# Kernel tuning notes

Measured on AMD Instinct MI355X. Metric: run time of the kernel, lower is better.

Reference implementation:

```python
import jax, jax.numpy as jnp
import numpy as np

B, L, IN_DIM, D_MODEL, N_LAYERS = 4, 1024, 64, 512, 3
D_INNER, STATE, DT_RANK, K = 1024, 16, 32, 4  # expand=2, dt_rank=d_model//16, conv kernel 4


def setup_inputs() -> dict:
    key = jax.random.key(0)
    ks = jax.random.split(key, 8)
    s = 0.02
    def rn(k, shp):
        return jax.random.normal(k, shp, jnp.float32) * s
    inp = {"x": jax.random.normal(ks[0], (B, L, IN_DIM), jnp.float32)}
    inp["input_w"] = rn(ks[1], (D_MODEL, IN_DIM)); inp["input_b"] = jnp.zeros((D_MODEL,), jnp.float32)
    inp["in_proj_w"] = rn(ks[2], (N_LAYERS, 2 * D_INNER, D_MODEL)); inp["in_proj_b"] = jnp.zeros((N_LAYERS, 2 * D_INNER), jnp.float32)
    inp["conv_w"] = rn(ks[3], (N_LAYERS, D_INNER, 1, K)); inp["conv_b"] = jnp.zeros((N_LAYERS, D_INNER), jnp.float32)
    inp["x_proj_w"] = rn(ks[4], (N_LAYERS, DT_RANK + 2 * STATE, D_INNER))
    inp["dt_proj_w"] = rn(ks[5], (N_LAYERS, D_INNER, DT_RANK)); inp["dt_proj_b"] = jnp.full((N_LAYERS, D_INNER), -4.0, jnp.float32)
    inp["A_log"] = jnp.tile(jnp.log(jnp.arange(1, STATE + 1, dtype=jnp.float32))[None, None, :], (N_LAYERS, D_INNER, 1))
    inp["D"] = jnp.ones((N_LAYERS, D_INNER), jnp.float32)
    inp["out_proj_w"] = rn(ks[6], (N_LAYERS, D_MODEL, D_INNER)); inp["out_proj_b"] = jnp.zeros((N_LAYERS, D_MODEL), jnp.float32)
    inp["ln_w"] = jnp.ones((N_LAYERS, D_MODEL), jnp.float32); inp["ln_b"] = jnp.zeros((N_LAYERS, D_MODEL), jnp.float32)
    return inp


def _layernorm(x, w, b):
    mu = jnp.mean(x, -1, keepdims=True)
    v = jnp.var(x, -1, keepdims=True)
    return (x - mu) * jax.lax.rsqrt(v + 1e-5) * w + b


def _mamba(u, iw, ib, cw, cb, xw, dw, db, A_log, Dp, ow, ob):
    # u: [B, L, d_model]
    xz = u @ iw.T + ib                          # [B, L, 2*d_inner]
    xp, z = jnp.split(xz, 2, axis=-1)
    # causal depthwise conv over time
    xc = jax.lax.conv_general_dilated(xp.transpose(0, 2, 1), cw, (1,), [(K - 1, 0)],
                                      feature_group_count=D_INNER,
                                      dimension_numbers=("NCH", "OIH", "NCH")) + cb[None, :, None]
    xc = jax.nn.silu(xc).transpose(0, 2, 1)     # [B, L, d_inner]
    proj = xc @ xw.T                            # [B, L, dt_rank + 2*N]
    dtl = proj[..., :DT_RANK]
    Bm = proj[..., DT_RANK:DT_RANK + STATE]
    Cm = proj[..., DT_RANK + STATE:]
    dt = jax.nn.softplus(dtl @ dw.T + db)       # [B, L, d_inner]
    A = -jnp.exp(A_log)                         # [d_inner, N]

    def step(h, t):
        dt_t, B_t, C_t, x_t = t                 # [B,d], [B,N], [B,N], [B,d]
        h = h * jnp.exp(dt_t[..., None] * A) + (dt_t * x_t)[..., None] * B_t[:, None, :]
        return h, jnp.einsum("bdn,bn->bd", h, C_t)

    h0 = jnp.zeros((u.shape[0], D_INNER, STATE), u.dtype)
    _, ys = jax.lax.scan(step, h0, (dt.transpose(1, 0, 2), Bm.transpose(1, 0, 2),
                                    Cm.transpose(1, 0, 2), xc.transpose(1, 0, 2)))
    y = ys.transpose(1, 0, 2) + xc * Dp
    y = y * jax.nn.silu(z)
    return y @ ow.T + ob


def reference(x, input_w, input_b, in_proj_w, in_proj_b, conv_w, conv_b, x_proj_w,
              dt_proj_w, dt_proj_b, A_log, D, out_proj_w, out_proj_b, ln_w, ln_b):
    h = x @ input_w.T + input_b                 # [B, L, d_model]
    for i in range(N_LAYERS):
        res = h
        h = _mamba(h, in_proj_w[i], in_proj_b[i], conv_w[i], conv_b[i], x_proj_w[i],
                   dt_proj_w[i], dt_proj_b[i], A_log[i], D[i], out_proj_w[i], out_proj_b[i])
        h = _layernorm(h + res, ln_w[i], ln_b[i])
    return h[:, -1, :]
```

## Files before the change

kernel.cpp:

```cpp
#include <hip/hip_runtime.h>
#include <hip/hip_bf16.h>
#include <cstddef>
#include <cstdint>

#define NB 4
#define NL 1024
#define IN_DIM 64
#define D_MODEL 512
#define N_LAYERS 3
#define D_INNER 1024
#define NSTATE 16
#define DT_RANK 32
#define KCONV 4
#define NROWS (NB * NL)
#define CHUNK 16
#define NCHUNK (NL / CHUNK)
#define LOG2E 1.4426950408889634f

typedef __attribute__((ext_vector_type(8))) short short8;
typedef __attribute__((ext_vector_type(4))) float f32x4;
typedef __attribute__((ext_vector_type(4))) unsigned short us4;
typedef unsigned short ushort_t;

__device__ __forceinline__ ushort_t f2b1(float x) {
  uint32_t u = __builtin_bit_cast(uint32_t, x);
  u += 0x7fffu + ((u >> 16) & 1u);
  return (ushort_t)(u >> 16);
}

__global__ __launch_bounds__(256) void f2b_kernel(
    const float* __restrict__ in, ushort_t* __restrict__ out, int n)
{
  const int i = (blockIdx.x * 256 + threadIdx.x) * 4;
  if (i >= n) return;
  const float4 v = *(const float4*)(in + i);
  us4 o;
  o.x = f2b1(v.x); o.y = f2b1(v.y); o.z = f2b1(v.z); o.w = f2b1(v.w);
  *(us4*)(out + i) = o;
}

template<int BM, int BN, int MF, int NF, int ACT, bool WF32, bool WB16>
__global__ __launch_bounds__(256) void gemm_mfma(
    const ushort_t* __restrict__ A, int lda,
    const ushort_t* __restrict__ W,
    const float* __restrict__ bias,
    float* __restrict__ Cf, ushort_t* __restrict__ Cb,
    int M, int N, int K)
{
  constexpr int LDSK = 48;
  constexpr int CA = BM / 64;
  constexpr int CB = BN / 64;
  __shared__ __align__(16) short sa[BM * LDSK];
  __shared__ __align__(16) short sb[BN * LDSK];

  const int tid = threadIdx.x;
  const int l = tid & 63;
  const int wid = tid >> 6;
  const int wrow = (wid >> 1) * (BM / 2);
  const int wcol = (wid & 1) * (BN / 2);
  const int m0 = blockIdx.y * BM;
  const int n0 = blockIdx.x * BN;

  f32x4 acc[MF][NF] = {};
  short8 ra[CA], rb[CB];

  auto loadg = [&](int k0) {
#pragma unroll
    for (int c = 0; c < CA; ++c) {
      const int chunk = c * 256 + tid;
      const int row = chunk >> 2, colb = chunk & 3;
      ra[c] = *(const short8*)(A + (size_t)(m0 + row) * lda + k0 + colb * 8);
    }
#pragma unroll
    for (int c = 0; c < CB; ++c) {
      const int chunk = c * 256 + tid;
      const int row = chunk >> 2, colb = chunk & 3;
      rb[c] = *(const short8*)(W + (size_t)(n0 + row) * K + k0 + colb * 8);
    }
  };
  auto store_lds = [&]() {
#pragma unroll
    for (int c = 0; c < CA; ++c) {
      const int chunk = c * 256 + tid;
      *(short8*)(sa + (chunk >> 2) * LDSK + (chunk & 3) * 8) = ra[c];
    }
#pragma unroll
    for (int c = 0; c < CB; ++c) {
      const int chunk = c * 256 + tid;
      *(short8*)(sb + (chunk >> 2) * LDSK + (chunk & 3) * 8) = rb[c];
    }
  };

  loadg(0);
  for (int k0 = 0; k0 < K; k0 += 32) {
    __syncthreads();
    store_lds();
    __syncthreads();
    if (k0 + 32 < K) loadg(k0 + 32);

    short8 af[MF], bfr[NF];
#pragma unroll
    for (int mi = 0; mi < MF; ++mi)
      af[mi] = *(const short8*)(sa + (wrow + mi * 16 + (l & 15)) * LDSK + (l >> 4) * 8);
#pragma unroll
    for (int nj = 0; nj < NF; ++nj)
      bfr[nj] = *(const short8*)(sb + (wcol + nj * 16 + (l & 15)) * LDSK + (l >> 4) * 8);
#pragma unroll
    for (int mi = 0; mi < MF; ++mi)
#pragma unroll
      for (int nj = 0; nj < NF; ++nj)
        acc[mi][nj] = __builtin_amdgcn_mfma_f32_16x16x32_bf16(
            af[mi], bfr[nj], acc[mi][nj], 0, 0, 0);
  }

#pragma unroll
  for (int nj = 0; nj < NF; ++nj) {
    const int col = n0 + wcol + nj * 16 + (l & 15);
    const float bv = bias ? bias[col] : 0.f;
#pragma unroll
    for (int mi = 0; mi < MF; ++mi) {
#pragma unroll
      for (int q = 0; q < 4; ++q) {
        const int row = m0 + wrow + mi * 16 + (l >> 4) * 4 + q;
        float v = acc[mi][nj][q] + bv;
        if (ACT == 1) v = (v > 20.f) ? v : log1pf(__expf(v));
        if (WF32) Cf[(size_t)row * N + col] = v;
        if (WB16) Cb[(size_t)row * N + col] = f2b1(v);
      }
    }
  }
}

__global__ __launch_bounds__(256) void conv_silu(
    const float* __restrict__ xz,
    const float* __restrict__ cw,
    const float* __restrict__ cb,
    float* __restrict__ xc,
    ushort_t* __restrict__ xcb)
{
  const int idx = blockIdx.x * 256 + threadIdx.x;
  const int d = idx & (D_INNER - 1);
  const int bt = idx >> 10;
  const int t = bt & (NL - 1);
  const int b = bt >> 10;

  float accv = cb[d];
#pragma unroll
  for (int j = 0; j < KCONV; ++j) {
    const int tt = t - (KCONV - 1) + j;
    if (tt >= 0)
      accv = fmaf(xz[((size_t)(b * NL + tt)) * (2 * D_INNER) + d], cw[d * KCONV + j], accv);
  }
  const float sig = 1.f / (1.f + __expf(-accv));
  const float val = accv * sig;
  xc[idx] = val;
  xcb[idx] = f2b1(val);
}

__global__ __launch_bounds__(256) void scan_phase1(
    const float* __restrict__ dt,
    const float* __restrict__ proj,
    const float* __restrict__ xc,
    const float* __restrict__ A_log,
    float* __restrict__ S_loc,
    float* __restrict__ sumdt)
{
  const int d = blockIdx.x * 256 + threadIdx.x;
  const int c = blockIdx.y;
  const int b = blockIdx.z;

  float A2[NSTATE];
#pragma unroll
  for (int n = 0; n < NSTATE; ++n)
    A2[n] = -__expf(A_log[d * NSTATE + n]) * LOG2E;

  float h[NSTATE];
#pragma unroll
  for (int n = 0; n < NSTATE; ++n) h[n] = 0.f;
  float sdt = 0.f;

  const int t0 = c * CHUNK;
#pragma unroll 4
  for (int tt = 0; tt < CHUNK; ++tt) {
    const size_t row = (size_t)(b * NL + t0 + tt);
    const float dtv = dt[row * D_INNER + d];
    const float xv = xc[row * D_INNER + d];
    const float* pr = proj + row * (DT_RANK + 2 * NSTATE);
    sdt += dtv;
    const float dx = dtv * xv;
#pragma unroll
    for (int n = 0; n < NSTATE; ++n)
      h[n] = fmaf(h[n], exp2f(dtv * A2[n]), dx * pr[DT_RANK + n]);
  }

  const size_t cbase = (size_t)(b * NCHUNK + c);
  sumdt[cbase * D_INNER + d] = sdt;
#pragma unroll
  for (int n = 0; n < NSTATE; ++n)
    S_loc[(cbase * NSTATE + n) * D_INNER + d] = h[n];
}

__global__ __launch_bounds__(256) void scan_carry(
    const float* __restrict__ S_loc,
    const float* __restrict__ sumdt,
    const float* __restrict__ A_log,
    float* __restrict__ H_in)
{
  const int idx = blockIdx.x * 256 + threadIdx.x;
  const int d = idx & (D_INNER - 1);
  const int n = (idx >> 10) & (NSTATE - 1);
  const int b = idx >> 14;

  const float A2n = -__expf(A_log[d * NSTATE + n]) * LOG2E;

  float H = 0.f;
  for (int c = 0; c < NCHUNK; ++c) {
    const size_t cbase = (size_t)(b * NCHUNK + c);
    H_in[(cbase * NSTATE + n) * D_INNER + d] = H;
    const float sdt = sumdt[cbase * D_INNER + d];
    H = fmaf(H, exp2f(A2n * sdt), S_loc[(cbase * NSTATE + n) * D_INNER + d]);
  }
}

__global__ __launch_bounds__(256) void scan_phase2(
    const float* __restrict__ dt,
    const float* __restrict__ proj,
    const float* __restrict__ xz,
    const float* __restrict__ A_log,
    const float* __restrict__ Dp,
    const float* __restrict__ H_in,
    const float* __restrict__ xc,
    ushort_t* __restrict__ yb)
{
  const int d = blockIdx.x * 256 + threadIdx.x;
  const int c = blockIdx.y;
  const int b = blockIdx.z;

  float A2[NSTATE];
#pragma unroll
  for (int n = 0; n < NSTATE; ++n)
    A2[n] = -__expf(A_log[d * NSTATE + n]) * LOG2E;

  const size_t cbase = (size_t)(b * NCHUNK + c);
  float h[NSTATE];
#pragma unroll
  for (int n = 0; n < NSTATE; ++n)
    h[n] = H_in[(cbase * NSTATE + n) * D_INNER + d];

  const float Dv = Dp[d];
  const int t0 = c * CHUNK;

#pragma unroll 4
  for (int tt = 0; tt < CHUNK; ++tt) {
    const size_t row = (size_t)(b * NL + t0 + tt);
    const size_t rd = row * D_INNER + d;
    const float dtv = dt[rd];
    const float xv = xc[rd];
    const float* pr = proj + row * (DT_RANK + 2 * NSTATE);
    const float dx = dtv * xv;
    float accv = 0.f;
#pragma unroll
    for (int n = 0; n < NSTATE; ++n) {
      h[n] = fmaf(h[n], exp2f(dtv * A2[n]), dx * pr[DT_RANK + n]);
      accv = fmaf(h[n], pr[DT_RANK + NSTATE + n], accv);
    }
    const float zv = xz[row * (2 * D_INNER) + D_INNER + d];
    float yv = fmaf(xv, Dv, accv);
    yv *= zv / (1.f + __expf(-zv));
    yb[rd] = f2b1(yv);
  }
}

__global__ __launch_bounds__(256) void add_ln(
    const float* __restrict__ x,
    const float* __restrict__ res,
    const float* __restrict__ w,
    const float* __restrict__ bln,
    float* __restrict__ out,
    ushort_t* __restrict__ outb)
{
  const int wave = threadIdx.x >> 6;
  const int lane = threadIdx.x & 63;
  const int row = blockIdx.x * 4 + wave;
  const float* xr = x + (size_t)row * D_MODEL;
  const float* rr = res + (size_t)row * D_MODEL;

  float v[8];
  float s = 0.f, s2 = 0.f;
#pragma unroll
  for (int i = 0; i < 8; ++i) {
    const float t = xr[lane + i * 64] + rr[lane + i * 64];
    v[i] = t; s += t; s2 = fmaf(t, t, s2);
  }
#pragma unroll
  for (int off = 32; off; off >>= 1) {
    s += __shfl_xor(s, off);
    s2 += __shfl_xor(s2, off);
  }
  const float mean = s * (1.f / D_MODEL);
  const float var = s2 * (1.f / D_MODEL) - mean * mean;
  const float rstd = rsqrtf(var + 1e-5f);
#pragma unroll
  for (int i = 0; i < 8; ++i) {
    const int c = lane + i * 64;
    const float o = (v[i] - mean) * rstd * w[c] + bln[c];
    out[(size_t)row * D_MODEL + c] = o;
    outb[(size_t)row * D_MODEL + c] = f2b1(o);
  }
}

__global__ __launch_bounds__(256) void extract_last(
    const float* __restrict__ h, float* __restrict__ out)
{
  const int idx = blockIdx.x * 256 + threadIdx.x;
  if (idx < NB * D_MODEL) {
    const int b = idx >> 9, j = idx & (D_MODEL - 1);
    out[idx] = h[((size_t)(b * NL + NL - 1)) * D_MODEL + j];
  }
}

extern "C" void kernel_launch(void* const* d_in, const int* in_sizes, int n_in,
                              void* d_out, int out_size, void* d_ws, size_t ws_size,
                              hipStream_t stream)
{
  const float* x         = (const float*)d_in[0];
  const float* input_w   = (const float*)d_in[1];
  const float* input_b   = (const float*)d_in[2];
  const float* in_proj_w = (const float*)d_in[3];
  const float* in_proj_b = (const float*)d_in[4];
  const float* conv_w    = (const float*)d_in[5];
  const float* conv_b    = (const float*)d_in[6];
  const float* x_proj_w  = (const float*)d_in[7];
  const float* dt_proj_w = (const float*)d_in[8];
  const float* dt_proj_b = (const float*)d_in[9];
  const float* A_log     = (const float*)d_in[10];
  const float* Dp        = (const float*)d_in[11];
  const float* out_proj_w= (const float*)d_in[12];
  const float* out_proj_b= (const float*)d_in[13];
  const float* ln_w      = (const float*)d_in[14];
  const float* ln_b      = (const float*)d_in[15];

  float* p = (float*)d_ws;
  float* h0   = p; p += (size_t)NROWS * D_MODEL;
  float* h1   = p; p += (size_t)NROWS * D_MODEL;
  float* xz   = p; p += (size_t)NROWS * 2 * D_INNER;
  float* xc   = p; p += (size_t)NROWS * D_INNER;
  float* proj = p; p += (size_t)NROWS * 64;
  float* dtb  = p; p += (size_t)NROWS * D_INNER;
  float* Sloc = p; p += (size_t)NB * NCHUNK * NSTATE * D_INNER;
  float* Hin  = p; p += (size_t)NB * NCHUNK * NSTATE * D_INNER;
  float* sdt  = p; p += (size_t)NB * NCHUNK * D_INNER;
  ushort_t* hb    = (ushort_t*)p; p += (size_t)NROWS * D_MODEL / 2;
  ushort_t* xb    = (ushort_t*)p; p += (size_t)NROWS * IN_DIM / 2;
  ushort_t* projb = (ushort_t*)p; p += (size_t)NROWS * 64 / 2;
  ushort_t* inwb  = (ushort_t*)p; p += (size_t)D_MODEL * IN_DIM / 2;
  ushort_t* iwb   = (ushort_t*)p; p += (size_t)N_LAYERS * 2 * D_INNER * D_MODEL / 2;
  ushort_t* xwb   = (ushort_t*)p; p += (size_t)N_LAYERS * 64 * D_INNER / 2;
  ushort_t* dwb   = (ushort_t*)p; p += (size_t)N_LAYERS * D_INNER * DT_RANK / 2;
  ushort_t* owb   = (ushort_t*)p; p += (size_t)N_LAYERS * D_MODEL * D_INNER / 2;
  ushort_t* yb  = (ushort_t*)Sloc;
  ushort_t* xcb = (ushort_t*)Hin;
  float* tmp = xz;

  auto cvt = [&](const float* src, ushort_t* dst, int n) {
    f2b_kernel<<<(n / 4 + 255) / 256, 256, 0, stream>>>(src, dst, n);
  };
  cvt(x, xb, NROWS * IN_DIM);
  cvt(input_w, inwb, D_MODEL * IN_DIM);
  cvt(in_proj_w, iwb, N_LAYERS * 2 * D_INNER * D_MODEL);
  cvt(x_proj_w, xwb, N_LAYERS * 64 * D_INNER);
  cvt(dt_proj_w, dwb, N_LAYERS * D_INNER * DT_RANK);
  cvt(out_proj_w, owb, N_LAYERS * D_MODEL * D_INNER);

  gemm_mfma<64, 128, 2, 4, 0, true, true>
      <<<dim3(D_MODEL / 128, NROWS / 64), 256, 0, stream>>>(
      xb, IN_DIM, inwb, input_b, h0, hb, NROWS, D_MODEL, IN_DIM);

  float* hc = h0;
  float* hn = h1;

  for (int l = 0; l < N_LAYERS; ++l) {
    const ushort_t* iw = iwb + (size_t)l * 2 * D_INNER * D_MODEL;
    const float* ib = in_proj_b + (size_t)l * 2 * D_INNER;
    const float* cw = conv_w    + (size_t)l * D_INNER * KCONV;
    const float* cb = conv_b    + (size_t)l * D_INNER;
    const ushort_t* xw = xwb + (size_t)l * 64 * D_INNER;
    const ushort_t* dw = dwb + (size_t)l * D_INNER * DT_RANK;
    const float* db = dt_proj_b + (size_t)l * D_INNER;
    const float* Al = A_log     + (size_t)l * D_INNER * NSTATE;
    const float* Dl = Dp        + (size_t)l * D_INNER;
    const ushort_t* ow = owb + (size_t)l * D_MODEL * D_INNER;
    const float* ob = out_proj_b+ (size_t)l * D_MODEL;
    const float* lw = ln_w      + (size_t)l * D_MODEL;
    const float* lb = ln_b      + (size_t)l * D_MODEL;

    gemm_mfma<128, 128, 4, 4, 0, true, false>
        <<<dim3(2 * D_INNER / 128, NROWS / 128), 256, 0, stream>>>(
        hb, D_MODEL, iw, ib, xz, nullptr, NROWS, 2 * D_INNER, D_MODEL);

    conv_silu<<<NROWS * D_INNER / 256, 256, 0, stream>>>(xz, cw, cb, xc, xcb);

    gemm_mfma<64, 64, 2, 2, 0, true, true>
        <<<dim3(1, NROWS / 64), 256, 0, stream>>>(
        xcb, D_INNER, xw, nullptr, proj, projb, NROWS, 64, D_INNER);

    gemm_mfma<128, 128, 4, 4, 1, true, false>
        <<<dim3(D_INNER / 128, NROWS / 128), 256, 0, stream>>>(
        projb, 64, dw, db, dtb, nullptr, NROWS, D_INNER, DT_RANK);

    scan_phase1<<<dim3(D_INNER / 256, NCHUNK, NB), 256, 0, stream>>>(
        dtb, proj, xc, Al, Sloc, sdt);
    scan_carry<<<(NB * NSTATE * D_INNER) / 256, 256, 0, stream>>>(
        Sloc, sdt, Al, Hin);
    scan_phase2<<<dim3(D_INNER / 256, NCHUNK, NB), 256, 0, stream>>>(
        dtb, proj, xz, Al, Dl, Hin, xc, yb);

    gemm_mfma<64, 128, 2, 4, 0, true, false>
        <<<dim3(D_MODEL / 128, NROWS / 64), 256, 0, stream>>>(
        yb, D_INNER, ow, ob, tmp, nullptr, NROWS, D_MODEL, D_INNER);

    add_ln<<<NROWS / 4, 256, 0, stream>>>(tmp, hc, lw, lb, hn, hb);

    float* t2 = hc; hc = hn; hn = t2;
  }

  extract_last<<<(NB * D_MODEL + 255) / 256, 256, 0, stream>>>(hc, (float*)d_out);
}
```

Baseline: 578.0 us.

## Fuse scan kernels, store intermediates as bf16, use direct LDS loads in GEMM

Merges the three chunked-scan kernels into one block-level kernel that does the inter-chunk carry in shared memory. Stores xz, xc, dt and y as bf16 instead of fp32 and vectorizes the conv. The GEMM now uses global_load_lds into unpadded LDS and drops its register prefetch, the weight conversions become one kernel, and last-row extraction moves into layernorm. This reduces memory traffic and launch count, at the cost of lower intermediate precision and less load/compute overlap in the GEMM.

```diff
diff --git a/kernel.cpp b/kernel.cpp
--- a/kernel.cpp
+++ b/kernel.cpp
@@ -27,16 +27,45 @@
   u += 0x7fffu + ((u >> 16) & 1u);
   return (ushort_t)(u >> 16);
 }
-
-__global__ __launch_bounds__(256) void f2b_kernel(
-    const float* __restrict__ in, ushort_t* __restrict__ out, int n)
-{
-  const int i = (blockIdx.x * 256 + threadIdx.x) * 4;
-  if (i >= n) return;
-  const float4 v = *(const float4*)(in + i);
+__device__ __forceinline__ float b2f(ushort_t u) {
+  return __builtin_bit_cast(float, (uint32_t)u << 16);
+}
+
+__device__ __forceinline__ void gload_lds16(const ushort_t* src, short* dst) {
+  __builtin_amdgcn_global_load_lds(
+      (const __attribute__((address_space(1))) uint32_t*)src,
+      (__attribute__((address_space(3))) uint32_t*)dst, 16, 0, 0);
+}
+
+#define E0 (NROWS * IN_DIM)
+#define E1 (D_MODEL * IN_DIM)
+#define E2 (N_LAYERS * 2 * D_INNER * D_MODEL)
+#define E3 (N_LAYERS * 64 * D_INNER)
+#define E4 (N_LAYERS * D_INNER * DT_RANK)
+#define E5 (N_LAYERS * D_MODEL * D_INNER)
+#define ETOT (E0 + E1 + E2 + E3 + E4 + E5)
+
+__global__ __launch_bounds__(256) void cvt_all(
+    const float* __restrict__ x, const float* __restrict__ inw,
+    const float* __restrict__ ipw, const float* __restrict__ xpw,
+    const float* __restrict__ dpw, const float* __restrict__ opw,
+    ushort_t* __restrict__ xb, ushort_t* __restrict__ inwb,
+    ushort_t* __restrict__ iwb, ushort_t* __restrict__ xwb,
+    ushort_t* __restrict__ dwb, ushort_t* __restrict__ owb)
+{
+  int i = (blockIdx.x * 256 + threadIdx.x) * 4;
+  if (i >= ETOT) return;
+  const float* src; ushort_t* dst; int off;
+  if      (i < E0)                  { src = x;   dst = xb;   off = i; }
+  else if (i < E0+E1)               { src = inw; dst = inwb; off = i - E0; }
+  else if (i < E0+E1+E2)            { src = ipw; dst = iwb;  off = i - (E0+E1); }
+  else if (i < E0+E1+E2+E3)         { src = xpw; dst = xwb;  off = i - (E0+E1+E2); }
+  else if (i < E0+E1+E2+E3+E4)      { src = dpw; dst = dwb;  off = i - (E0+E1+E2+E3); }
+  else                              { src = opw; dst = owb;  off = i - (E0+E1+E2+E3+E4); }
+  const float4 v = *(const float4*)(src + off);
   us4 o;
   o.x = f2b1(v.x); o.y = f2b1(v.y); o.z = f2b1(v.z); o.w = f2b1(v.w);
-  *(us4*)(out + i) = o;
+  *(us4*)(dst + off) = o;
 }
 
 template<int BM, int BN, int MF, int NF, int ACT, bool WF32, bool WB16>
@@ -47,11 +76,10 @@
     float* __restrict__ Cf, ushort_t* __restrict__ Cb,
     int M, int N, int K)
 {
-  constexpr int LDSK = 48;
   constexpr int CA = BM / 64;
   constexpr int CB = BN / 64;
-  __shared__ __align__(16) short sa[BM * LDSK];
-  __shared__ __align__(16) short sb[BN * LDSK];
+  __shared__ __align__(16) short sa[BM * 32];
+  __shared__ __align__(16) short sb[BN * 32];
 
   const int tid = threadIdx.x;
   const int l = tid & 63;
@@ -61,56 +89,42 @@
   const int m0 = blockIdx.y * BM;
   const int n0 = blockIdx.x * BN;
 
+  const int srow = l >> 2;
+  const int scol = (l & 3) * 8;
+
   f32x4 acc[MF][NF] = {};
-  short8 ra[CA], rb[CB];
-
-  auto loadg = [&](int k0) {
+
+  for (int k0 = 0; k0 < K; k0 += 32) {
 #pragma unroll
     for (int c = 0; c < CA; ++c) {
-      const int chunk = c * 256 + tid;
-      const int row = chunk >> 2, colb = chunk & 3;
-      ra[c] = *(const short8*)(A + (size_t)(m0 + row) * lda + k0 + colb * 8);
+      short* dst = sa + (c * 4 + wid) * 512;
+      const ushort_t* src =
+          A + (size_t)(m0 + (c * 4 + wid) * 16 + srow) * lda + k0 + scol;
+      gload_lds16(src, dst);
     }
 #pragma unroll
     for (int c = 0; c < CB; ++c) {
-      const int chunk = c * 256 + tid;
-      const int row = chunk >> 2, colb = chunk & 3;
-      rb[c] = *(const short8*)(W + (size_t)(n0 + row) * K + k0 + colb * 8);
-    }
-  };
-  auto store_lds = [&]() {
-#pragma unroll
-    for (int c = 0; c < CA; ++c) {
-      const int chunk = c * 256 + tid;
-      *(short8*)(sa + (chunk >> 2) * LDSK + (chunk & 3) * 8) = ra[c];
-    }
-#pragma unroll
-    for (int c = 0; c < CB; ++c) {
-      const int chunk = c * 256 + tid;
-      *(short8*)(sb + (chunk >> 2) * LDSK + (chunk & 3) * 8) = rb[c];
-    }
-  };
-
-  loadg(0);
-  for (int k0 = 0; k0 < K; k0 += 32) {
+      short* dst = sb + (c * 4 + wid) * 512;
+      const ushort_t* src =
+          W + (size_t)(n0 + (c * 4 + wid) * 16 + srow) * K + k0 + scol;
+      gload_lds16(src, dst);
+    }
     __syncthreads();
-    store_lds();
-    __syncthreads();
-    if (k0 + 32 < K) loadg(k0 + 32);
 
     short8 af[MF], bfr[NF];
 #pragma unroll
     for (int mi = 0; mi < MF; ++mi)
-      af[mi] = *(const short8*)(sa + (wrow + mi * 16 + (l & 15)) * LDSK + (l >> 4) * 8);
+      af[mi] = *(const short8*)(sa + (wrow + mi * 16 + (l & 15)) * 32 + (l >> 4) * 8);
 #pragma unroll
     for (int nj = 0; nj < NF; ++nj)
-      bfr[nj] = *(const short8*)(sb + (wcol + nj * 16 + (l & 15)) * LDSK + (l >> 4) * 8);
+      bfr[nj] = *(const short8*)(sb + (wcol + nj * 16 + (l & 15)) * 32 + (l >> 4) * 8);
 #pragma unroll
     for (int mi = 0; mi < MF; ++mi)
 #pragma unroll
       for (int nj = 0; nj < NF; ++nj)
         acc[mi][nj] = __builtin_amdgcn_mfma_f32_16x16x32_bf16(
             af[mi], bfr[nj], acc[mi][nj], 0, 0, 0);
+    __syncthreads();
   }
 
 #pragma unroll
@@ -132,139 +146,138 @@
 }
 
 __global__ __launch_bounds__(256) void conv_silu(
-    const float* __restrict__ xz,
+    const ushort_t* __restrict__ xzb,
     const float* __restrict__ cw,
     const float* __restrict__ cb,
-    float* __restrict__ xc,
     ushort_t* __restrict__ xcb)
 {
   const int idx = blockIdx.x * 256 + threadIdx.x;
-  const int d = idx & (D_INNER - 1);
-  const int bt = idx >> 10;
+  const int d4 = (idx & (D_INNER / 4 - 1)) * 4;
+  const int bt = idx >> 8;
   const int t = bt & (NL - 1);
   const int b = bt >> 10;
 
-  float accv = cb[d];
+  float acc4[4];
+  {
+    const float4 cbv = *(const float4*)(cb + d4);
+    acc4[0] = cbv.x; acc4[1] = cbv.y; acc4[2] = cbv.z; acc4[3] = cbv.w;
+  }
+  float wv[4][4];
+#pragma unroll
+  for (int i = 0; i < 4; ++i) {
+    const float4 w = *(const float4*)(cw + (size_t)(d4 + i) * KCONV);
+    wv[i][0] = w.x; wv[i][1] = w.y; wv[i][2] = w.z; wv[i][3] = w.w;
+  }
 #pragma unroll
   for (int j = 0; j < KCONV; ++j) {
     const int tt = t - (KCONV - 1) + j;
-    if (tt >= 0)
-      accv = fmaf(xz[((size_t)(b * NL + tt)) * (2 * D_INNER) + d], cw[d * KCONV + j], accv);
-  }
-  const float sig = 1.f / (1.f + __expf(-accv));
-  const float val = accv * sig;
-  xc[idx] = val;
-  xcb[idx] = f2b1(val);
-}
-
-__global__ __launch_bounds__(256) void scan_phase1(
-    const float* __restrict__ dt,
+    if (tt >= 0) {
+      const us4 xv = *(const us4*)(xzb + (size_t)(b * NL + tt) * (2 * D_INNER) + d4);
+      acc4[0] = fmaf(b2f(xv.x), wv[0][j], acc4[0]);
+      acc4[1] = fmaf(b2f(xv.y), wv[1][j], acc4[1]);
+      acc4[2] = fmaf(b2f(xv.z), wv[2][j], acc4[2]);
+      acc4[3] = fmaf(b2f(xv.w), wv[3][j], acc4[3]);
+    }
+  }
+  us4 o;
+#pragma unroll
+  for (int i = 0; i < 4; ++i) {
+    const float s = acc4[i] / (1.f + __expf(-acc4[i]));
+    ((ushort_t*)&o)[i] = f2b1(s);
+  }
+  *(us4*)(xcb + (size_t)idx * 4) = o;
+}
+
+__global__ __launch_bounds__(256) void scan_fused(
+    const ushort_t* __restrict__ dtb,
     const float* __restrict__ proj,
-    const float* __restrict__ xc,
+    const ushort_t* __restrict__ xcb,
+    const ushort_t* __restrict__ xzb,
     const float* __restrict__ A_log,
-    float* __restrict__ S_loc,
-    float* __restrict__ sumdt)
-{
-  const int d = blockIdx.x * 256 + threadIdx.x;
-  const int c = blockIdx.y;
-  const int b = blockIdx.z;
+    const float* __restrict__ Dp,
+    ushort_t* __restrict__ yb)
+{
+  __shared__ float S_lds[NCHUNK][4][NSTATE + 1];
+  __shared__ float H_lds[NCHUNK][4][NSTATE + 1];
+  __shared__ float sdt_lds[NCHUNK][4];
+
+  const int tid = threadIdx.x;
+  const int c = tid >> 2;
+  const int dl = tid & 3;
+  const int d = blockIdx.x * 4 + dl;
+  const int b = blockIdx.y;
 
   float A2[NSTATE];
 #pragma unroll
   for (int n = 0; n < NSTATE; ++n)
     A2[n] = -__expf(A_log[d * NSTATE + n]) * LOG2E;
 
+  const int t0 = c * CHUNK;
   float h[NSTATE];
 #pragma unroll
   for (int n = 0; n < NSTATE; ++n) h[n] = 0.f;
   float sdt = 0.f;
 
-  const int t0 = c * CHUNK;
-#pragma unroll 4
   for (int tt = 0; tt < CHUNK; ++tt) {
     const size_t row = (size_t)(b * NL + t0 + tt);
-    const float dtv = dt[row * D_INNER + d];
-    const float xv = xc[row * D_INNER + d];
-    const float* pr = proj + row * (DT_RANK + 2 * NSTATE);
+    const float dtv = b2f(dtb[row * D_INNER + d]);
+    const float xv = b2f(xcb[row * D_INNER + d]);
+    const float* pr = proj + row * 64;
+    float Bv[NSTATE];
+    *(float4*)(Bv)      = *(const float4*)(pr + 32);
+    *(float4*)(Bv + 4)  = *(const float4*)(pr + 36);
+    *(float4*)(Bv + 8)  = *(const float4*)(pr + 40);
+    *(float4*)(Bv + 12) = *(const float4*)(pr + 44);
     sdt += dtv;
     const float dx = dtv * xv;
 #pragma unroll
     for (int n = 0; n < NSTATE; ++n)
-      h[n] = fmaf(h[n], exp2f(dtv * A2[n]), dx * pr[DT_RANK + n]);
-  }
-
-  const size_t cbase = (size_t)(b * NCHUNK + c);
-  sumdt[cbase * D_INNER + d] = sdt;
-#pragma unroll
-  for (int n = 0; n < NSTATE; ++n)
-    S_loc[(cbase * NSTATE + n) * D_INNER + d] = h[n];
-}
-
-__global__ __launch_bounds__(256) void scan_carry(
-    const float* __restrict__ S_loc,
-    const float* __restrict__ sumdt,
-    const float* __restrict__ A_log,
-    float* __restrict__ H_in)
-{
-  const int idx = blockIdx.x * 256 + threadIdx.x;
-  const int d = idx & (D_INNER - 1);
-  const int n = (idx >> 10) & (NSTATE - 1);
-  const int b = idx >> 14;
-
-  const float A2n = -__expf(A_log[d * NSTATE + n]) * LOG2E;
-
-  float H = 0.f;
-  for (int c = 0; c < NCHUNK; ++c) {
-    const size_t cbase = (size_t)(b * NCHUNK + c);
-    H_in[(cbase * NSTATE + n) * D_INNER + d] = H;
-    const float sdt = sumdt[cbase * D_INNER + d];
-    H = fmaf(H, exp2f(A2n * sdt), S_loc[(cbase * NSTATE + n) * D_INNER + d]);
-  }
-}
-
-__global__ __launch_bounds__(256) void scan_phase2(
-    const float* __restrict__ dt,
-    const float* __restrict__ proj,
-    const float* __restrict__ xz,
-    const float* __restrict__ A_log,
-    const float* __restrict__ Dp,
-    const float* __restrict__ H_in,
-    const float* __restrict__ xc,
-    ushort_t* __restrict__ yb)
-{
-  const int d = blockIdx.x * 256 + threadIdx.x;
-  const int c = blockIdx.y;
-  const int b = blockIdx.z;
-
-  float A2[NSTATE];
-#pragma unroll
-  for (int n = 0; n < NSTATE; ++n)
-    A2[n] = -__expf(A_log[d * NSTATE + n]) * LOG2E;
-
-  const size_t cbase = (size_t)(b * NCHUNK + c);
-  float h[NSTATE];
-#pragma unroll
-  for (int n = 0; n < NSTATE; ++n)
-    h[n] = H_in[(cbase * NSTATE + n) * D_INNER + d];
-
+      h[n] = fmaf(h[n], exp2f(dtv * A2[n]), dx * Bv[n]);
+  }
+  sdt_lds[c][dl] = sdt;
+#pragma unroll
+  for (int n = 0; n < NSTATE; ++n) S_lds[c][dl][n] = h[n];
+  __syncthreads();
+
+  if (tid < 64) {
+    const int dl2 = tid >> 4;
+    const int n2 = tid & 15;
+    const float A2n = -__expf(A_log[(blockIdx.x * 4 + dl2) * NSTATE + n2]) * LOG2E;
+    float H = 0.f;
+    for (int cc = 0; cc < NCHUNK; ++cc) {
+      H_lds[cc][dl2][n2] = H;
+      H = fmaf(H, exp2f(A2n * sdt_lds[cc][dl2]), S_lds[cc][dl2][n2]);
+    }
+  }
+  __syncthreads();
+
+#pragma unroll
+  for (int n = 0; n < NSTATE; ++n) h[n] = H_lds[c][dl][n];
   const float Dv = Dp[d];
-  const int t0 = c * CHUNK;
-
-#pragma unroll 4
+
   for (int tt = 0; tt < CHUNK; ++tt) {
     const size_t row = (size_t)(b * NL + t0 + tt);
     const size_t rd = row * D_INNER + d;
-    const float dtv = dt[rd];
-    const float xv = xc[rd];
-    const float* pr = proj + row * (DT_RANK + 2 * NSTATE);
+    const float dtv = b2f(dtb[rd]);
+    const float xv = b2f(xcb[rd]);
+    const float* pr = proj + row * 64;
+    float Bv[NSTATE], Cv[NSTATE];
+    *(float4*)(Bv)      = *(const float4*)(pr + 32);
+    *(float4*)(Bv + 4)  = *(const float4*)(pr + 36);
+    *(float4*)(Bv + 8)  = *(const float4*)(pr + 40);
+    *(float4*)(Bv + 12) = *(const float4*)(pr + 44);
+    *(float4*)(Cv)      = *(const float4*)(pr + 48);
+    *(float4*)(Cv + 4)  = *(const float4*)(pr + 52);
+    *(float4*)(Cv + 8)  = *(const float4*)(pr + 56);
+    *(float4*)(Cv + 12) = *(const float4*)(pr + 60);
     const float dx = dtv * xv;
     float accv = 0.f;
 #pragma unroll
     for (int n = 0; n < NSTATE; ++n) {
-      h[n] = fmaf(h[n], exp2f(dtv * A2[n]), dx * pr[DT_RANK + n]);
-      accv = fmaf(h[n], pr[DT_RANK + NSTATE + n], accv);
-    }
-    const float zv = xz[row * (2 * D_INNER) + D_INNER + d];
+      h[n] = fmaf(h[n], exp2f(dtv * A2[n]), dx * Bv[n]);
+      accv = fmaf(h[n], Cv[n], accv);
+    }
+    const float zv = b2f(xzb[row * (2 * D_INNER) + D_INNER + d]);
     float yv = fmaf(xv, Dv, accv);
     yv *= zv / (1.f + __expf(-zv));
     yb[rd] = f2b1(yv);
@@ -277,7 +290,8 @@
     const float* __restrict__ w,
     const float* __restrict__ bln,
     float* __restrict__ out,
-    ushort_t* __restrict__ outb)
+    ushort_t* __restrict__ outb,
+    float* __restrict__ out2)
 {
   const int wave = threadIdx.x >> 6;
   const int lane = threadIdx.x & 63;
@@ -300,22 +314,14 @@
   const float mean = s * (1.f / D_MODEL);
   const float var = s2 * (1.f / D_MODEL) - mean * mean;
   const float rstd = rsqrtf(var + 1e-5f);
+  const bool last_t = (row & (NL - 1)) == (NL - 1);
 #pragma unroll
   for (int i = 0; i < 8; ++i) {
     const int c = lane + i * 64;
     const float o = (v[i] - mean) * rstd * w[c] + bln[c];
     out[(size_t)row * D_MODEL + c] = o;
     outb[(size_t)row * D_MODEL + c] = f2b1(o);
-  }
-}
-
-__global__ __launch_bounds__(256) void extract_last(
-    const float* __restrict__ h, float* __restrict__ out)
-{
-  const int idx = blockIdx.x * 256 + threadIdx.x;
-  if (idx < NB * D_MODEL) {
-    const int b = idx >> 9, j = idx & (D_MODEL - 1);
-    out[idx] = h[((size_t)(b * NL + NL - 1)) * D_MODEL + j];
+    if (out2 && last_t) out2[(size_t)(row >> 10) * D_MODEL + c] = o;
   }
 }
 
@@ -343,37 +349,28 @@
   float* p = (float*)d_ws;
   float* h0   = p; p += (size_t)NROWS * D_MODEL;
   float* h1   = p; p += (size_t)NROWS * D_MODEL;
-  float* xz   = p; p += (size_t)NROWS * 2 * D_INNER;
-  float* xc   = p; p += (size_t)NROWS * D_INNER;
+  float* tmp  = p; p += (size_t)NROWS * D_MODEL;
   float* proj = p; p += (size_t)NROWS * 64;
-  float* dtb  = p; p += (size_t)NROWS * D_INNER;
-  float* Sloc = p; p += (size_t)NB * NCHUNK * NSTATE * D_INNER;
-  float* Hin  = p; p += (size_t)NB * NCHUNK * NSTATE * D_INNER;
-  float* sdt  = p; p += (size_t)NB * NCHUNK * D_INNER;
-  ushort_t* hb    = (ushort_t*)p; p += (size_t)NROWS * D_MODEL / 2;
-  ushort_t* xb    = (ushort_t*)p; p += (size_t)NROWS * IN_DIM / 2;
-  ushort_t* projb = (ushort_t*)p; p += (size_t)NROWS * 64 / 2;
-  ushort_t* inwb  = (ushort_t*)p; p += (size_t)D_MODEL * IN_DIM / 2;
-  ushort_t* iwb   = (ushort_t*)p; p += (size_t)N_LAYERS * 2 * D_INNER * D_MODEL / 2;
-  ushort_t* xwb   = (ushort_t*)p; p += (size_t)N_LAYERS * 64 * D_INNER / 2;
-  ushort_t* dwb   = (ushort_t*)p; p += (size_t)N_LAYERS * D_INNER * DT_RANK / 2;
-  ushort_t* owb   = (ushort_t*)p; p += (size_t)N_LAYERS * D_MODEL * D_INNER / 2;
-  ushort_t* yb  = (ushort_t*)Sloc;
-  ushort_t* xcb = (ushort_t*)Hin;
-  float* tmp = xz;
-
-  auto cvt = [&](const float* src, ushort_t* dst, int n) {
-    f2b_kernel<<<(n / 4 + 255) / 256, 256, 0, stream>>>(src, dst, n);
-  };
-  cvt(x, xb, NROWS * IN_DIM);
-  cvt(input_w, inwb, D_MODEL * IN_DIM);
-  cvt(in_proj_w, iwb, N_LAYERS * 2 * D_INNER * D_MODEL);
-  cvt(x_proj_w, xwb, N_LAYERS * 64 * D_INNER);
-  cvt(dt_proj_w, dwb, N_LAYERS * D_INNER * DT_RANK);
-  cvt(out_proj_w, owb, N_LAYERS * D_MODEL * D_INNER);
-
-  gemm_mfma<64, 128, 2, 4, 0, true, true>
-      <<<dim3(D_MODEL / 128, NROWS / 64), 256, 0, stream>>>(
+  ushort_t* q = (ushort_t*)p;
+  ushort_t* xzb   = q; q += (size_t)NROWS * 2 * D_INNER;
+  ushort_t* xcb   = q; q += (size_t)NROWS * D_INNER;
+  ushort_t* dtbb  = q; q += (size_t)NROWS * D_INNER;
+  ushort_t* projb = q; q += (size_t)NROWS * 64;
+  ushort_t* yb    = q; q += (size_t)NROWS * D_INNER;
+  ushort_t* hb    = q; q += (size_t)NROWS * D_MODEL;
+  ushort_t* xb    = q; q += (size_t)E0;
+  ushort_t* inwb  = q; q += (size_t)E1;
+  ushort_t* iwb   = q; q += (size_t)E2;
+  ushort_t* xwb   = q; q += (size_t)E3;
+  ushort_t* dwb   = q; q += (size_t)E4;
+  ushort_t* owb   = q; q += (size_t)E5;
+
+  cvt_all<<<(ETOT / 4 + 255) / 256, 256, 0, stream>>>(
+      x, input_w, in_proj_w, x_proj_w, dt_proj_w, out_proj_w,
+      xb, inwb, iwb, xwb, dwb, owb);
+
+  gemm_mfma<64, 64, 2, 2, 0, true, true>
+      <<<dim3(D_MODEL / 64, NROWS / 64), 256, 0, stream>>>(
       xb, IN_DIM, inwb, input_b, h0, hb, NROWS, D_MODEL, IN_DIM);
 
   float* hc = h0;
@@ -394,35 +391,31 @@
     const float* lw = ln_w      + (size_t)l * D_MODEL;
     const float* lb = ln_b      + (size_t)l * D_MODEL;
 
-    gemm_mfma<128, 128, 4, 4, 0, true, false>
+    gemm_mfma<128, 128, 4, 4, 0, false, true>
         <<<dim3(2 * D_INNER / 128, NROWS / 128), 256, 0, stream>>>(
-        hb, D_MODEL, iw, ib, xz, nullptr, NROWS, 2 * D_INNER, D_MODEL);
-
-    conv_silu<<<NROWS * D_INNER / 256, 256, 0, stream>>>(xz, cw, cb, xc, xcb);
+        hb, D_MODEL, iw, ib, nullptr, xzb, NROWS, 2 * D_INNER, D_MODEL);
+
+    conv_silu<<<NROWS * D_INNER / 4 / 256, 256, 0, stream>>>(xzb, cw, cb, xcb);
 
     gemm_mfma<64, 64, 2, 2, 0, true, true>
         <<<dim3(1, NROWS / 64), 256, 0, stream>>>(
         xcb, D_INNER, xw, nullptr, proj, projb, NROWS, 64, D_INNER);
 
-    gemm_mfma<128, 128, 4, 4, 1, true, false>
+    gemm_mfma<128, 128, 4, 4, 1, false, true>
         <<<dim3(D_INNER / 128, NROWS / 128), 256, 0, stream>>>(
-        projb, 64, dw, db, dtb, nullptr, NROWS, D_INNER, DT_RANK);
-
-    scan_phase1<<<dim3(D_INNER / 256, NCHUNK, NB), 256, 0, stream>>>(
-        dtb, proj, xc, Al, Sloc, sdt);
-    scan_carry<<<(NB * NSTATE * D_INNER) / 256, 256, 0, stream>>>(
-        Sloc, sdt, Al, Hin);
-    scan_phase2<<<dim3(D_INNER / 256, NCHUNK, NB), 256, 0, stream>>>(
-        dtb, proj, xz, Al, Dl, Hin, xc, yb);
-
-    gemm_mfma<64, 128, 2, 4, 0, true, false>
-        <<<dim3(D_MODEL / 128, NROWS / 64), 256, 0, stream>>>(
+        projb, 64, dw, db, nullptr, dtbb, NROWS, D_INNER, DT_RANK);
+
+    scan_fused<<<dim3(D_INNER / 4, NB), 256, 0, stream>>>(
+        dtbb, proj, xcb, xzb, Al, Dl, yb);
+
+    gemm_mfma<64, 64, 2, 2, 0, true, false>
+        <<<dim3(D_MODEL / 64, NROWS / 64), 256, 0, stream>>>(
         yb, D_INNER, ow, ob, tmp, nullptr, NROWS, D_MODEL, D_INNER);
 
-    add_ln<<<NROWS / 4, 256, 0, stream>>>(tmp, hc, lw, lb, hn, hb);
+    add_ln<<<NROWS / 4, 256, 0, stream>>>(
+        tmp, hc, lw, lb, hn, hb,
+        (l == N_LAYERS - 1) ? (float*)d_out : nullptr);
 
     float* t2 = hc; hc = hn; hn = t2;
   }
-
-  extract_last<<<(NB * D_MODEL + 255) / 256, 256, 0, stream>>>(hc, (float*)d_out);
-}
+}
```

Result: slower. 634.8 us (+9.8%).
